# Optimization experiments

Measured on AMD Instinct MI355X. Metric: run time of the kernel, lower is better.

The kernel has to match this reference:

```python
import jax, jax.numpy as jnp
import numpy as np

N = 50000  # num nodes
E = 800000  # num edges


def gcn_layer(x, W, b, senders, receivers, snorm, rnorm):
    # jraph.GraphConvolution(Dense, add_self_edges=False, symmetric_normalization=True)
    h = x @ W + b                       # [N, F_out] dense transform
    h = h * snorm[:, None]              # scale by rsqrt(max(sender_degree, 1))
    agg = jax.ops.segment_sum(h[senders], receivers, num_segments=N)  # scatter-add over edges
    return agg * rnorm[:, None]         # scale by rsqrt(max(receiver_degree, 1))


def setup_inputs() -> dict:
    key = jax.random.key(0)
    ks = jax.random.split(key, 6)
    nodes = jax.random.normal(ks[0], (N, 128), jnp.float32)
    senders = jax.random.randint(ks[1], (E,), 0, N)
    receivers = jax.random.randint(ks[2], (E,), 0, N)

    def dense(k, fin, fout):
        kw, _ = jax.random.split(k)
        scale = 1.0 / np.sqrt(fin).astype(np.float32)
        W = jax.random.uniform(kw, (fin, fout), jnp.float32, -scale, scale)
        b = jnp.zeros((fout,), jnp.float32)
        return W, b

    W1, b1 = dense(ks[3], 128, 256)
    W2, b2 = dense(ks[4], 256, 256)
    W3, b3 = dense(ks[5], 256, 128)
    return dict(nodes=nodes, senders=senders, receivers=receivers,
                W1=W1, b1=b1, W2=W2, b2=b2, W3=W3, b3=b3)


def reference(nodes, senders, receivers, W1, b1, W2, b2, W3, b3):
    ones = jnp.ones((E,), nodes.dtype)
    sdeg = jax.ops.segment_sum(ones, senders, num_segments=N)
    rdeg = jax.ops.segment_sum(ones, receivers, num_segments=N)
    snorm = jax.lax.rsqrt(jnp.maximum(sdeg, 1.0))
    rnorm = jax.lax.rsqrt(jnp.maximum(rdeg, 1.0))

    x = nodes
    for W, b in ((W1, b1), (W2, b2), (W3, b3)):
        x = gcn_layer(x, W, b, senders, receivers, snorm, rnorm)
        x = jax.nn.relu(x)  # activation applied after every layer, incl. last
        # dropout is deterministic (eval mode) -> identity
    return x
```

## Files before the change

### kernel.cpp

```cpp
#include <hip/hip_runtime.h>
#include <hip/hip_fp16.h>


typedef __attribute__((ext_vector_type(8))) short short8;
typedef __attribute__((ext_vector_type(4))) float f32x4;

#define DCAP 64
#define PBITS 8
#define EPB 4096

static __device__ __forceinline__ float reluf(float x){ return x > 0.f ? x : 0.f; }

static __device__ __forceinline__ unsigned short bf16_rn(float v){
    unsigned u = __float_as_uint(v);
    unsigned r = u + 0x7FFFu + ((u >> 16) & 1u);
    return (unsigned short)(r >> 16);
}
static __device__ __forceinline__ void split2(float v, unsigned short& h, unsigned short& l){
    unsigned short hh = bf16_rn(v);
    float hf = __uint_as_float(((unsigned)hh) << 16);
    h = hh;
    l = bf16_rn(v - hf);
}
static __device__ __forceinline__ unsigned short f2h(float v){
    return __half_as_ushort(__float2half(v));
}
static __device__ __forceinline__ float h2f(unsigned short u){
    return __half2float(__ushort_as_half(u));
}

static __device__ __forceinline__ void gload_lds16(const void* g, void* lds){
    __builtin_amdgcn_global_load_lds((const __attribute__((address_space(1))) unsigned int*)g,
                                     (__attribute__((address_space(3))) unsigned int*)lds, 16, 0, 0);
}


__global__ __launch_bounds__(256)
void p1_hist(const int* __restrict__ snd, const int* __restrict__ rcv,
             int* __restrict__ cntR, int* __restrict__ cntS, int e, int NP, int NB)
{
    __shared__ int hR[256], hS[256];
    int t = threadIdx.x;
    hR[t] = 0; hS[t] = 0;
    __syncthreads();
    int base = blockIdx.x * EPB;
#pragma unroll
    for (int k = 0; k < EPB / 256; ++k) {
        int i = base + k * 256 + t;
        if (i < e) {
            atomicAdd(&hR[rcv[i] >> PBITS], 1);
            atomicAdd(&hS[snd[i] >> PBITS], 1);
        }
    }
    __syncthreads();
    if (t < NP) {
        cntR[t * NB + blockIdx.x] = hR[t];
        cntS[t * NB + blockIdx.x] = hS[t];
    }
}

__global__ __launch_bounds__(256)
void p2a_scanpart(const int* __restrict__ cntR, int* __restrict__ withinR, int* __restrict__ totR,
                  const int* __restrict__ cntS, int* __restrict__ withinS, int* __restrict__ totS,
                  int NB)
{
    __shared__ int s[256];
    int t = threadIdx.x;
    int p = blockIdx.x;
    int v = (t < NB) ? cntR[p * NB + t] : 0;
    s[t] = v;
    __syncthreads();
    for (int d = 1; d < 256; d <<= 1) {
        int x = (t >= d) ? s[t - d] : 0;
        __syncthreads();
        s[t] += x;
        __syncthreads();
    }
    if (t < NB) withinR[p * NB + t] = s[t] - v;
    if (t == 255) totR[p] = s[255];
    __syncthreads();
    v = (t < NB) ? cntS[p * NB + t] : 0;
    s[t] = v;
    __syncthreads();
    for (int d = 1; d < 256; d <<= 1) {
        int x = (t >= d) ? s[t - d] : 0;
        __syncthreads();
        s[t] += x;
        __syncthreads();
    }
    if (t < NB) withinS[p * NB + t] = s[t] - v;
    if (t == 255) totS[p] = s[255];
}

__global__ __launch_bounds__(256)
void p2b_scantops(const int* __restrict__ totR, int* __restrict__ pbaseR,
                  const int* __restrict__ totS, int* __restrict__ pbaseS, int NP)
{
    __shared__ int s[256];
    int t = threadIdx.x;
    int v = (t < NP) ? totR[t] : 0;
    s[t] = v;
    __syncthreads();
    for (int d = 1; d < 256; d <<= 1) {
        int x = (t >= d) ? s[t - d] : 0;
        __syncthreads();
        s[t] += x;
        __syncthreads();
    }
    if (t < NP) pbaseR[t] = s[t] - v;
    if (t == 255) pbaseR[NP] = s[255];
    __syncthreads();
    v = (t < NP) ? totS[t] : 0;
    s[t] = v;
    __syncthreads();
    for (int d = 1; d < 256; d <<= 1) {
        int x = (t >= d) ? s[t - d] : 0;
        __syncthreads();
        s[t] += x;
        __syncthreads();
    }
    if (t < NP) pbaseS[t] = s[t] - v;
    if (t == 255) pbaseS[NP] = s[255];
}

__global__ __launch_bounds__(256)
void p3_scatter(const int* __restrict__ snd, const int* __restrict__ rcv,
                const int* __restrict__ pbaseR, const int* __restrict__ withinR,
                const int* __restrict__ pbaseS, const int* __restrict__ withinS,
                unsigned int* __restrict__ eP, unsigned short* __restrict__ sP,
                int e, int NP, int NB)
{
    __shared__ int bR[256], cR[256], bS[256], cS[256];
    int t = threadIdx.x;
    if (t < NP) {
        bR[t] = pbaseR[t] + withinR[t * NB + blockIdx.x];
        bS[t] = pbaseS[t] + withinS[t * NB + blockIdx.x];
    }
    cR[t] = 0; cS[t] = 0;
    __syncthreads();
    int base = blockIdx.x * EPB;
#pragma unroll
    for (int k = 0; k < EPB / 256; ++k) {
        int i = base + k * 256 + t;
        if (i < e) {
            int s = snd[i], r = rcv[i];
            int pr = r >> PBITS, ps = s >> PBITS;
            int rk = atomicAdd(&cR[pr], 1);
            eP[bR[pr] + rk] = ((unsigned)r << 16) | (unsigned)s;
            int sk = atomicAdd(&cS[ps], 1);
            sP[bS[ps] + sk] = (unsigned short)s;
        }
    }
}

__global__ __launch_bounds__(256)
void p4_csr(const unsigned int* __restrict__ eP, const int* __restrict__ pbaseR,
            unsigned short* __restrict__ esrc, int* __restrict__ rcntP,
            float* __restrict__ rnormP, int* __restrict__ inv, int n)
{
    __shared__ unsigned short buck[256 * DCAP];
    __shared__ int cnt[256];
    __shared__ int hist[64], hbase[64], cur[64], sc[64];
    int t = threadIdx.x;
    cnt[t] = 0;
    if (t < 64) { hist[t] = 0; cur[t] = 0; }
    __syncthreads();
    int p = blockIdx.x;
    int lo = pbaseR[p];
    int hi = pbaseR[p + 1];
    for (int i = lo + t; i < hi; i += 256) {
        unsigned u = eP[i];
        int lr = (u >> 16) & 255;
        int slot = atomicAdd(&cnt[lr], 1);
        if (slot < DCAP) buck[lr * DCAP + slot] = (unsigned short)(u & 0xFFFFu);
    }
    __syncthreads();
    int nvalid = min(256, n - p * 256);
    int deg = (t < nvalid) ? min(cnt[t], 63) : -1;
    if (deg >= 0) atomicAdd(&hist[deg], 1);
    __syncthreads();
    int hv = (t < 64) ? hist[t] : 0;
    if (t < 64) sc[t] = hv;
    __syncthreads();
    for (int d = 1; d < 64; d <<= 1) {
        int x = (t < 64 && t >= d) ? sc[t - d] : 0;
        __syncthreads();
        if (t < 64) sc[t] += x;
        __syncthreads();
    }
    if (t < 64) hbase[t] = sc[t] - hv;
    __syncthreads();
    if (deg >= 0) {
        int slot = p * 256 + hbase[deg] + atomicAdd(&cur[deg], 1);
        inv[p * 256 + t] = slot;
        int full = cnt[t];
        rcntP[slot] = min(full, DCAP);
        rnormP[slot] = rsqrtf(fmaxf((float)full, 1.0f));
        unsigned short* dst = esrc + (size_t)slot * DCAP;
        const unsigned short* src = buck + t * DCAP;
#pragma unroll
        for (int k = 0; k < DCAP / 8; ++k)
            *(short8*)(dst + k * 8) = *(const short8*)(src + k * 8);
    }
}

__global__ __launch_bounds__(256)
void p4b_sdeg(const unsigned short* __restrict__ sP, const int* __restrict__ pbaseS,
              float* __restrict__ snormN, int n)
{
    __shared__ int cnt[256];
    int t = threadIdx.x;
    cnt[t] = 0;
    __syncthreads();
    int p = blockIdx.x;
    int lo = pbaseS[p];
    int hi = pbaseS[p + 1];
    for (int i = lo + t; i < hi; i += 256)
        atomicAdd(&cnt[sP[i] & 255], 1);
    __syncthreads();
    int g = p * 256 + t;
    if (g < n) snormN[g] = rsqrtf(fmaxf((float)cnt[t], 1.0f));
}

__global__ __launch_bounds__(256)
void p5_remap(unsigned short* __restrict__ esrc, const int* __restrict__ rcntP,
              const int* __restrict__ inv, const float* __restrict__ snormN,
              float* __restrict__ snormP, int n)
{
    int i = blockIdx.x * 256 + threadIdx.x;
    if (i < n) snormP[inv[i]] = snormN[i];
    if (i < n * DCAP) {
        int slot = i >> 6, j = i & 63;
        if (j < rcntP[slot]) esrc[i] = (unsigned short)inv[esrc[i]];
    }
}

__global__ void conv_h_kernel(const float* __restrict__ x, unsigned short* __restrict__ y,
                              const int* __restrict__ inv, int n)
{
    int i = blockIdx.x * 256 + threadIdx.x;
    if (i >= n * 32) return;
    int node = i >> 5, c4 = i & 31;
    float4 v = *(const float4*)(x + (size_t)node * 128 + c4 * 4);
    ushort4 o = make_ushort4(f2h(v.x), f2h(v.y), f2h(v.z), f2h(v.w));
    *(ushort4*)(y + (size_t)inv[node] * 128 + c4 * 4) = o;
}

__global__ void wsplit_kernel(const float* __restrict__ W, unsigned short* __restrict__ Th,
                              unsigned short* __restrict__ Tl, int K, int N)
{
    int i = blockIdx.x * 256 + threadIdx.x;
    if (i >= K * N) return;
    int k = i / N, c = i % N;
    unsigned short h, l;
    split2(W[i], h, l);
    Th[c * K + k] = h;
    Tl[c * K + k] = l;
}

template<int K, int NOUT, int OMODE, bool APAIR>
__global__ __launch_bounds__(256)
void mfma_gemm(const unsigned short* __restrict__ A_g,
               const unsigned short* __restrict__ Bh_g, const unsigned short* __restrict__ Bl_g,
               const float* __restrict__ bias, const float* __restrict__ rs,
               const float* __restrict__ bs, float* __restrict__ Ht,
               unsigned short* __restrict__ Ot, int n)
{
    __shared__ unsigned short smem[4 * 128 * 32];
    unsigned short* Ah = smem;
    unsigned short* Al = smem + 4096;
    unsigned short* Bh = smem + 8192;
    unsigned short* Bl = smem + 12288;

    const int tid = threadIdx.x;
    const int wid = tid >> 6, lane = tid & 63;
    const int wr = (wid >> 1) * 64, wc = (wid & 1) * 64;
    const int r0 = blockIdx.x * 128, c0 = blockIdx.y * 128;

    f32x4 acc[4][4];
#pragma unroll
    for (int m = 0; m < 4; ++m)
#pragma unroll
        for (int q = 0; q < 4; ++q) acc[m][q] = (f32x4){0.f, 0.f, 0.f, 0.f};

    const int ks = lane >> 4, lr = lane & 15;
    const int ASTRIDE = APAIR ? 2 * K : K;

    for (int k0 = 0; k0 < K; k0 += 32) {
#pragma unroll
        for (int c = 0; c < 2; ++c) {
            int i = tid + c * 256;
            int row = i >> 2, p = i & 3;
            int g = p ^ ((row >> 1) & 3);
            int ar = r0 + row; if (ar >= n) ar = n - 1;
            size_t aoff = (size_t)ar * ASTRIDE + k0 + g * 8;
            gload_lds16(A_g + aoff, Ah + i * 8);
            if (APAIR) gload_lds16(A_g + aoff + K, Al + i * 8);
            size_t boff = (size_t)(c0 + row) * K + k0 + g * 8;
            gload_lds16(Bh_g + boff, Bh + i * 8);
            gload_lds16(Bl_g + boff, Bl + i * 8);
        }
        __syncthreads();

        short8 a_h[4], a_l[4], b_h[4], b_l[4];
#pragma unroll
        for (int m = 0; m < 4; ++m) {
            int r = wr + m * 16 + lr;
            int slot = ks ^ ((r >> 1) & 3);
            a_h[m] = *(const short8*)(Ah + r * 32 + slot * 8);
            if (APAIR) a_l[m] = *(const short8*)(Al + r * 32 + slot * 8);
        }
#pragma unroll
        for (int q = 0; q < 4; ++q) {
            int r = wc + q * 16 + lr;
            int slot = ks ^ ((r >> 1) & 3);
            b_h[q] = *(const short8*)(Bh + r * 32 + slot * 8);
            b_l[q] = *(const short8*)(Bl + r * 32 + slot * 8);
        }
#pragma unroll
        for (int m = 0; m < 4; ++m)
#pragma unroll
            for (int q = 0; q < 4; ++q) {
                acc[m][q] = __builtin_amdgcn_mfma_f32_16x16x32_bf16(a_h[m], b_h[q], acc[m][q], 0, 0, 0);
                acc[m][q] = __builtin_amdgcn_mfma_f32_16x16x32_bf16(a_h[m], b_l[q], acc[m][q], 0, 0, 0);
                if (APAIR)
                    acc[m][q] = __builtin_amdgcn_mfma_f32_16x16x32_bf16(a_l[m], b_h[q], acc[m][q], 0, 0, 0);
            }
        __syncthreads();
    }

    const int lq = lane >> 4;
    float* eps = (float*)smem;
    unsigned short* eph = smem;
    unsigned short* epl = smem + 32 * 136;

#pragma unroll
    for (int m = 0; m < 4; ++m) {
        __syncthreads();
#pragma unroll
        for (int j = 0; j < 4; ++j) {
            int gr = r0 + wr + m * 16 + lq * 4 + j;
            int cr = (wid >> 1) * 16 + lq * 4 + j;
            float rsv, bsv;
            if (gr < n) { rsv = rs[gr]; bsv = bs[gr]; } else { rsv = 0.f; bsv = 0.f; }
#pragma unroll
            for (int q = 0; q < 4; ++q) {
                int col = wc + q * 16 + lr;
                float v = acc[m][q][j] * rsv + bias[c0 + col] * bsv;
                if (OMODE == 1) {
                    v = reluf(v);
                    unsigned short h, l;
                    split2(v, h, l);
                    eph[cr * 136 + col] = h;
                    epl[cr * 136 + col] = l;
                } else if (OMODE == 2) {
                    eph[cr * 136 + col] = f2h(v);
                } else if (OMODE == 3) {
                    eph[cr * 136 + col] = bf16_rn(reluf(v));
                } else {
                    eps[cr * 132 + col] = v;
                }
            }
        }
        __syncthreads();
        int rr = tid >> 3, seg = tid & 7;
        int gr = r0 + (rr >> 4) * 64 + m * 16 + (rr & 15);
        if (gr < n) {
            if (OMODE == 1) {
                unsigned short* dst = Ot + (size_t)gr * (2 * NOUT) + c0 + seg * 16;
#pragma unroll
                for (int k = 0; k < 2; ++k) {
                    *(short8*)(dst + k * 8) = *(const short8*)(eph + rr * 136 + seg * 16 + k * 8);
                    *(short8*)(dst + NOUT + k * 8) = *(const short8*)(epl + rr * 136 + seg * 16 + k * 8);
                }
            } else if (OMODE == 2 || OMODE == 3) {
                unsigned short* dst = Ot + (size_t)gr * NOUT + c0 + seg * 16;
#pragma unroll
                for (int k = 0; k < 2; ++k)
                    *(short8*)(dst + k * 8) = *(const short8*)(eph + rr * 136 + seg * 16 + k * 8);
            } else {
                float* dst = Ht + (size_t)gr * NOUT + c0 + seg * 16;
#pragma unroll
                for (int k = 0; k < 4; ++k)
                    *(float4*)(dst + k * 4) = *(const float4*)(eps + rr * 132 + seg * 16 + k * 4);
            }
        }
    }
}


__global__ __launch_bounds__(256)
void gather1_t(const unsigned short* __restrict__ Nh, const int* __restrict__ rcntP,
               const unsigned short* __restrict__ esrc, const float* __restrict__ snormP,
               const float* __restrict__ rnormP,
               unsigned short* __restrict__ G, float* __restrict__ bs, int n)
{
    int g = blockIdx.x * 256 + threadIdx.x;
    int node = g >> 4, lane = g & 15;
    if (node >= n) return;
    int col = blockIdx.y * 64 + lane * 4;
    const unsigned short* Nc = Nh + col;
    int e0 = node * DCAP;
    int e1 = e0 + rcntP[node];
    float a0 = 0, a1 = 0, a2 = 0, a3 = 0, gs = 0;
    int e = e0;
    for (; e + 4 <= e1; e += 4) {
        int s0 = esrc[e], s1 = esrc[e + 1], s2 = esrc[e + 2], s3 = esrc[e + 3];
        float n0 = snormP[s0], n1 = snormP[s1], n2 = snormP[s2], n3 = snormP[s3];
        ushort4 v0 = *(const ushort4*)(Nc + (size_t)s0 * 128);
        ushort4 v1 = *(const ushort4*)(Nc + (size_t)s1 * 128);
        ushort4 v2 = *(const ushort4*)(Nc + (size_t)s2 * 128);
        ushort4 v3 = *(const ushort4*)(Nc + (size_t)s3 * 128);
        a0 += h2f(v0.x) * n0 + h2f(v1.x) * n1 + h2f(v2.x) * n2 + h2f(v3.x) * n3;
        a1 += h2f(v0.y) * n0 + h2f(v1.y) * n1 + h2f(v2.y) * n2 + h2f(v3.y) * n3;
        a2 += h2f(v0.z) * n0 + h2f(v1.z) * n1 + h2f(v2.z) * n2 + h2f(v3.z) * n3;
        a3 += h2f(v0.w) * n0 + h2f(v1.w) * n1 + h2f(v2.w) * n2 + h2f(v3.w) * n3;
        gs += n0 + n1 + n2 + n3;
    }
    for (; e < e1; ++e) {
        int s = esrc[e];
        float ns = snormP[s];
        ushort4 v = *(const ushort4*)(Nc + (size_t)s * 128);
        a0 += h2f(v.x) * ns; a1 += h2f(v.y) * ns; a2 += h2f(v.z) * ns; a3 += h2f(v.w) * ns;
        gs += ns;
    }
    ushort4 o = make_ushort4(bf16_rn(a0), bf16_rn(a1), bf16_rn(a2), bf16_rn(a3));
    *(ushort4*)(G + (size_t)node * 128 + col) = o;
    if (blockIdx.y == 0 && lane == 0) bs[node] = gs * rnormP[node];
}

__global__ __launch_bounds__(256)
void gather2_t(const unsigned short* __restrict__ Hh, const int* __restrict__ rcntP,
               const unsigned short* __restrict__ esrc, const float* __restrict__ rnormP,
               unsigned short* __restrict__ X3, int n)
{
    int g = blockIdx.x * 256 + threadIdx.x;
    int node = g >> 4, lane = g & 15;
    if (node >= n) return;
    int col = blockIdx.y * 64 + lane * 4;
    const unsigned short* Hc = Hh + col;
    int e0 = node * DCAP;
    int e1 = e0 + rcntP[node];
    float a0 = 0, a1 = 0, a2 = 0, a3 = 0;
    int e = e0;
    for (; e + 4 <= e1; e += 4) {
        int s0 = esrc[e], s1 = esrc[e + 1], s2 = esrc[e + 2], s3 = esrc[e + 3];
        ushort4 v0 = *(const ushort4*)(Hc + (size_t)s0 * 256);
        ushort4 v1 = *(const ushort4*)(Hc + (size_t)s1 * 256);
        ushort4 v2 = *(const ushort4*)(Hc + (size_t)s2 * 256);
        ushort4 v3 = *(const ushort4*)(Hc + (size_t)s3 * 256);
        a0 += h2f(v0.x) + h2f(v1.x) + h2f(v2.x) + h2f(v3.x);
        a1 += h2f(v0.y) + h2f(v1.y) + h2f(v2.y) + h2f(v3.y);
        a2 += h2f(v0.z) + h2f(v1.z) + h2f(v2.z) + h2f(v3.z);
        a3 += h2f(v0.w) + h2f(v1.w) + h2f(v2.w) + h2f(v3.w);
    }
    for (; e < e1; ++e) {
        int s = esrc[e];
        ushort4 v = *(const ushort4*)(Hc + (size_t)s * 256);
        a0 += h2f(v.x); a1 += h2f(v.y); a2 += h2f(v.z); a3 += h2f(v.w);
    }
    float rn = rnormP[node];
    ushort4 o = make_ushort4(bf16_rn(reluf(a0 * rn)), bf16_rn(reluf(a1 * rn)),
                             bf16_rn(reluf(a2 * rn)), bf16_rn(reluf(a3 * rn)));
    *(ushort4*)(X3 + (size_t)node * 256 + col) = o;
}

__global__ __launch_bounds__(256)
void gather3_t(const unsigned short* __restrict__ Hh, const int* __restrict__ rcntP,
               const unsigned short* __restrict__ esrc, const float* __restrict__ rnormP,
               const int* __restrict__ inv, float* __restrict__ out, int n)
{
    int g = blockIdx.x * 256 + threadIdx.x;
    int node = g >> 4, lane = g & 15;
    if (node >= n) return;
    int iv = inv[node];
    int col = blockIdx.y * 64 + lane * 4;
    const unsigned short* Hc = Hh + col;
    int e0 = iv * DCAP;
    int e1 = e0 + rcntP[iv];
    float a0 = 0, a1 = 0, a2 = 0, a3 = 0;
    int e = e0;
    for (; e + 4 <= e1; e += 4) {
        int s0 = esrc[e], s1 = esrc[e + 1], s2 = esrc[e + 2], s3 = esrc[e + 3];
        ushort4 v0 = *(const ushort4*)(Hc + (size_t)s0 * 128);
        ushort4 v1 = *(const ushort4*)(Hc + (size_t)s1 * 128);
        ushort4 v2 = *(const ushort4*)(Hc + (size_t)s2 * 128);
        ushort4 v3 = *(const ushort4*)(Hc + (size_t)s3 * 128);
        a0 += h2f(v0.x) + h2f(v1.x) + h2f(v2.x) + h2f(v3.x);
        a1 += h2f(v0.y) + h2f(v1.y) + h2f(v2.y) + h2f(v3.y);
        a2 += h2f(v0.z) + h2f(v1.z) + h2f(v2.z) + h2f(v3.z);
        a3 += h2f(v0.w) + h2f(v1.w) + h2f(v2.w) + h2f(v3.w);
    }
    for (; e < e1; ++e) {
        int s = esrc[e];
        ushort4 v = *(const ushort4*)(Hc + (size_t)s * 128);
        a0 += h2f(v.x); a1 += h2f(v.y); a2 += h2f(v.z); a3 += h2f(v.w);
    }
    float rn = rnormP[iv];
    float4 o = { reluf(a0 * rn), reluf(a1 * rn), reluf(a2 * rn), reluf(a3 * rn) };
    *(float4*)(out + (size_t)node * 128 + col) = o;
}


extern "C" void kernel_launch(void* const* d_in, const int* in_sizes, int n_in,
                              void* d_out, int out_size, void* d_ws, size_t ws_size,
                              hipStream_t stream)
{
    const float* nodes = (const float*)d_in[0];
    const int*   snd   = (const int*)d_in[1];
    const int*   rcv   = (const int*)d_in[2];
    const float* W1    = (const float*)d_in[3];
    const float* b1    = (const float*)d_in[4];
    const float* W2    = (const float*)d_in[5];
    const float* b2    = (const float*)d_in[6];
    const float* W3    = (const float*)d_in[7];
    const float* b3    = (const float*)d_in[8];
    const int n = in_sizes[0] / 128;
    const int e = in_sizes[1];
    float* out = (float*)d_out;

    const int NP = (n + 255) >> 8;
    const int NB = (e + EPB - 1) / EPB;

    char* w = (char*)d_ws;
    size_t o = 0;
    auto alloc = [&](size_t b){ size_t p = o; o += (b + 255) & ~(size_t)255; return p; };
    unsigned short* Hh   = (unsigned short*)(w + alloc((size_t)n * 256 * 2));
    unsigned short* X2   = (unsigned short*)(w + alloc((size_t)n * 256 * 2));
    char*           bufA = w + alloc((size_t)n * 512 * 2);
    unsigned short* Nh   = (unsigned short*)bufA;
    unsigned short* G    = (unsigned short*)(bufA + (size_t)n * 128 * 2);
    unsigned short* X3   = (unsigned short*)bufA;
    unsigned short* Wt1h = (unsigned short*)(w + alloc(256 * 128 * 2));
    unsigned short* Wt1l = (unsigned short*)(w + alloc(256 * 128 * 2));
    unsigned short* Wt2h = (unsigned short*)(w + alloc(256 * 256 * 2));
    unsigned short* Wt2l = (unsigned short*)(w + alloc(256 * 256 * 2));
    unsigned short* Wt3h = (unsigned short*)(w + alloc(128 * 256 * 2));
    unsigned short* Wt3l = (unsigned short*)(w + alloc(128 * 256 * 2));
    float* bsb   = (float*)(w + alloc((size_t)n * 4));
    int*   cntR   = (int*)(w + alloc((size_t)NP * NB * 4));
    int*   withinR= (int*)(w + alloc((size_t)NP * NB * 4));
    int*   cntS   = (int*)(w + alloc((size_t)NP * NB * 4));
    int*   withinS= (int*)(w + alloc((size_t)NP * NB * 4));
    int*   totR   = (int*)(w + alloc((size_t)NP * 4));
    int*   totS   = (int*)(w + alloc((size_t)NP * 4));
    int*   pbaseR = (int*)(w + alloc((size_t)(NP + 1) * 4));
    int*   pbaseS = (int*)(w + alloc((size_t)(NP + 1) * 4));
    unsigned int*   eP   = (unsigned int*)  (w + alloc((size_t)e * 4));
    unsigned short* sP   = (unsigned short*)(w + alloc((size_t)e * 2));
    unsigned short* esrc = (unsigned short*)(w + alloc((size_t)n * DCAP * 2));
    int*   rcntP = (int*)  (w + alloc((size_t)n * 4));
    int*   inv   = (int*)  (w + alloc((size_t)n * 4));
    float* snormN= (float*)(w + alloc((size_t)n * 4));
    float* snormP= (float*)(w + alloc((size_t)n * 4));
    float* rnormP= (float*)(w + alloc((size_t)n * 4));

    p1_hist<<<NB, 256, 0, stream>>>(snd, rcv, cntR, cntS, e, NP, NB);
    p2a_scanpart<<<NP, 256, 0, stream>>>(cntR, withinR, totR, cntS, withinS, totS, NB);
    p2b_scantops<<<1, 256, 0, stream>>>(totR, pbaseR, totS, pbaseS, NP);
    p3_scatter<<<NB, 256, 0, stream>>>(snd, rcv, pbaseR, withinR, pbaseS, withinS, eP, sP, e, NP, NB);
    p4_csr<<<NP, 256, 0, stream>>>(eP, pbaseR, esrc, rcntP, rnormP, inv, n);
    p4b_sdeg<<<NP, 256, 0, stream>>>(sP, pbaseS, snormN, n);
    p5_remap<<<((size_t)n * DCAP + 255) / 256, 256, 0, stream>>>(esrc, rcntP, inv, snormN, snormP, n);

    conv_h_kernel<<<((size_t)n * 32 + 255) / 256, 256, 0, stream>>>(nodes, Nh, inv, n);
    wsplit_kernel<<<(128 * 256 + 255) / 256, 256, 0, stream>>>(W1, Wt1h, Wt1l, 128, 256);
    wsplit_kernel<<<(256 * 256 + 255) / 256, 256, 0, stream>>>(W2, Wt2h, Wt2l, 256, 256);
    wsplit_kernel<<<(256 * 128 + 255) / 256, 256, 0, stream>>>(W3, Wt3h, Wt3l, 256, 128);

    int gb = (n + 127) / 128;
    int lb = ((size_t)n * 16 + 255) / 256;

    gather1_t<<<dim3(lb, 2), 256, 0, stream>>>(Nh, rcntP, esrc, snormP, rnormP, G, bsb, n);
    mfma_gemm<128, 256, 3, false><<<dim3(gb, 2), 256, 0, stream>>>(G, Wt1h, Wt1l, b1, rnormP, bsb,
                                                                   (float*)nullptr, X2, n);
    mfma_gemm<256, 256, 2, false><<<dim3(gb, 2), 256, 0, stream>>>(X2, Wt2h, Wt2l, b2, snormP, snormP,
                                                                   (float*)nullptr, Hh, n);
    gather2_t<<<dim3(lb, 4), 256, 0, stream>>>(Hh, rcntP, esrc, rnormP, X3, n);
    mfma_gemm<256, 128, 2, false><<<dim3(gb, 1), 256, 0, stream>>>(X3, Wt3h, Wt3l, b3, snormP, snormP,
                                                                   (float*)nullptr, Hh, n);
    gather3_t<<<dim3(lb, 2), 256, 0, stream>>>(Hh, rcntP, esrc, rnormP, inv, out, n);
}
```

Measured before the change: 267.0 us.

## Fuse preprocessing kernels and widen gathers to 16-byte loads per lane

Folds the sender-degree pass into the CSR build kernel, merges the fp32-to-half node conversion into the remap kernel, and combines the three weight-split launches into one, cutting kernel launch count. The three gather kernels now load 8 halfs per lane with short8 instead of 4, so each lane covers twice the columns and the grid's y dimension is halved or removed. This lowers launch overhead and repeated index/norm loads per edge, but gives fewer threads in flight to hide gather latency.

```diff
diff --git a/kernel.cpp b/kernel.cpp
--- a/kernel.cpp
+++ b/kernel.cpp
@@ -155,8 +155,10 @@
 
 __global__ __launch_bounds__(256)
 void p4_csr(const unsigned int* __restrict__ eP, const int* __restrict__ pbaseR,
+            const unsigned short* __restrict__ sP, const int* __restrict__ pbaseS,
             unsigned short* __restrict__ esrc, int* __restrict__ rcntP,
-            float* __restrict__ rnormP, int* __restrict__ inv, int n)
+            float* __restrict__ rnormP, int* __restrict__ inv,
+            float* __restrict__ snormN, int n)
 {
     __shared__ unsigned short buck[256 * DCAP];
     __shared__ int cnt[256];
@@ -177,6 +179,7 @@
     __syncthreads();
     int nvalid = min(256, n - p * 256);
     int deg = (t < nvalid) ? min(cnt[t], 63) : -1;
+    int full = (t < nvalid) ? cnt[t] : 0;
     if (deg >= 0) atomicAdd(&hist[deg], 1);
     __syncthreads();
     int hv = (t < 64) ? hist[t] : 0;
@@ -193,7 +196,6 @@
     if (deg >= 0) {
         int slot = p * 256 + hbase[deg] + atomicAdd(&cur[deg], 1);
         inv[p * 256 + t] = slot;
-        int full = cnt[t];
         rcntP[slot] = min(full, DCAP);
         rnormP[slot] = rsqrtf(fmaxf((float)full, 1.0f));
         unsigned short* dst = esrc + (size_t)slot * DCAP;
@@ -202,58 +204,53 @@
         for (int k = 0; k < DCAP / 8; ++k)
             *(short8*)(dst + k * 8) = *(const short8*)(src + k * 8);
     }
-}
-
-__global__ __launch_bounds__(256)
-void p4b_sdeg(const unsigned short* __restrict__ sP, const int* __restrict__ pbaseS,
-              float* __restrict__ snormN, int n)
-{
-    __shared__ int cnt[256];
-    int t = threadIdx.x;
+    __syncthreads();
     cnt[t] = 0;
     __syncthreads();
-    int p = blockIdx.x;
-    int lo = pbaseS[p];
-    int hi = pbaseS[p + 1];
-    for (int i = lo + t; i < hi; i += 256)
+    int lo2 = pbaseS[p];
+    int hi2 = pbaseS[p + 1];
+    for (int i = lo2 + t; i < hi2; i += 256)
         atomicAdd(&cnt[sP[i] & 255], 1);
     __syncthreads();
-    int g = p * 256 + t;
-    if (g < n) snormN[g] = rsqrtf(fmaxf((float)cnt[t], 1.0f));
-}
-
-__global__ __launch_bounds__(256)
-void p5_remap(unsigned short* __restrict__ esrc, const int* __restrict__ rcntP,
-              const int* __restrict__ inv, const float* __restrict__ snormN,
-              float* __restrict__ snormP, int n)
+    if (t < nvalid) snormN[p * 256 + t] = rsqrtf(fmaxf((float)cnt[t], 1.0f));
+}
+
+__global__ __launch_bounds__(256)
+void p5_finish(unsigned short* __restrict__ esrc, const int* __restrict__ rcntP,
+               const int* __restrict__ inv, const float* __restrict__ snormN,
+               float* __restrict__ snormP, const float* __restrict__ nodes,
+               unsigned short* __restrict__ Nh, int n)
 {
     int i = blockIdx.x * 256 + threadIdx.x;
     if (i < n) snormP[inv[i]] = snormN[i];
+    if (i < n * 32) {
+        int node = i >> 5, c4 = i & 31;
+        float4 v = *(const float4*)(nodes + (size_t)node * 128 + c4 * 4);
+        ushort4 o = make_ushort4(f2h(v.x), f2h(v.y), f2h(v.z), f2h(v.w));
+        *(ushort4*)(Nh + (size_t)inv[node] * 128 + c4 * 4) = o;
+    }
     if (i < n * DCAP) {
         int slot = i >> 6, j = i & 63;
         if (j < rcntP[slot]) esrc[i] = (unsigned short)inv[esrc[i]];
     }
 }
 
-__global__ void conv_h_kernel(const float* __restrict__ x, unsigned short* __restrict__ y,
-                              const int* __restrict__ inv, int n)
+__global__ __launch_bounds__(256)
+void wsplit_all(const float* __restrict__ W1, const float* __restrict__ W2,
+                const float* __restrict__ W3,
+                unsigned short* __restrict__ T1h, unsigned short* __restrict__ T1l,
+                unsigned short* __restrict__ T2h, unsigned short* __restrict__ T2l,
+                unsigned short* __restrict__ T3h, unsigned short* __restrict__ T3l)
 {
     int i = blockIdx.x * 256 + threadIdx.x;
-    if (i >= n * 32) return;
-    int node = i >> 5, c4 = i & 31;
-    float4 v = *(const float4*)(x + (size_t)node * 128 + c4 * 4);
-    ushort4 o = make_ushort4(f2h(v.x), f2h(v.y), f2h(v.z), f2h(v.w));
-    *(ushort4*)(y + (size_t)inv[node] * 128 + c4 * 4) = o;
-}
-
-__global__ void wsplit_kernel(const float* __restrict__ W, unsigned short* __restrict__ Th,
-                              unsigned short* __restrict__ Tl, int K, int N)
-{
-    int i = blockIdx.x * 256 + threadIdx.x;
-    if (i >= K * N) return;
-    int k = i / N, c = i % N;
+    const float* W; unsigned short *Th, *Tl; int K, N, idx;
+    if (i < 32768)       { W = W1; Th = T1h; Tl = T1l; K = 128; N = 256; idx = i; }
+    else if (i < 98304)  { W = W2; Th = T2h; Tl = T2l; K = 256; N = 256; idx = i - 32768; }
+    else if (i < 131072) { W = W3; Th = T3h; Tl = T3l; K = 256; N = 128; idx = i - 98304; }
+    else return;
+    int k = idx / N, c = idx % N;
     unsigned short h, l;
-    split2(W[i], h, l);
+    split2(W[idx], h, l);
     Th[c * K + k] = h;
     Tl[c * K + k] = l;
 }
@@ -398,35 +395,39 @@
     int g = blockIdx.x * 256 + threadIdx.x;
     int node = g >> 4, lane = g & 15;
     if (node >= n) return;
-    int col = blockIdx.y * 64 + lane * 4;
+    int col = lane * 8;
     const unsigned short* Nc = Nh + col;
     int e0 = node * DCAP;
     int e1 = e0 + rcntP[node];
-    float a0 = 0, a1 = 0, a2 = 0, a3 = 0, gs = 0;
+    float a[8] = {0, 0, 0, 0, 0, 0, 0, 0};
+    float gs = 0;
     int e = e0;
     for (; e + 4 <= e1; e += 4) {
         int s0 = esrc[e], s1 = esrc[e + 1], s2 = esrc[e + 2], s3 = esrc[e + 3];
         float n0 = snormP[s0], n1 = snormP[s1], n2 = snormP[s2], n3 = snormP[s3];
-        ushort4 v0 = *(const ushort4*)(Nc + (size_t)s0 * 128);
-        ushort4 v1 = *(const ushort4*)(Nc + (size_t)s1 * 128);
-        ushort4 v2 = *(const ushort4*)(Nc + (size_t)s2 * 128);
-        ushort4 v3 = *(const ushort4*)(Nc + (size_t)s3 * 128);
-        a0 += h2f(v0.x) * n0 + h2f(v1.x) * n1 + h2f(v2.x) * n2 + h2f(v3.x) * n3;
-        a1 += h2f(v0.y) * n0 + h2f(v1.y) * n1 + h2f(v2.y) * n2 + h2f(v3.y) * n3;
-        a2 += h2f(v0.z) * n0 + h2f(v1.z) * n1 + h2f(v2.z) * n2 + h2f(v3.z) * n3;
-        a3 += h2f(v0.w) * n0 + h2f(v1.w) * n1 + h2f(v2.w) * n2 + h2f(v3.w) * n3;
+        short8 v0 = *(const short8*)(Nc + (size_t)s0 * 128);
+        short8 v1 = *(const short8*)(Nc + (size_t)s1 * 128);
+        short8 v2 = *(const short8*)(Nc + (size_t)s2 * 128);
+        short8 v3 = *(const short8*)(Nc + (size_t)s3 * 128);
+#pragma unroll
+        for (int k = 0; k < 8; ++k)
+            a[k] += h2f((unsigned short)v0[k]) * n0 + h2f((unsigned short)v1[k]) * n1
+                  + h2f((unsigned short)v2[k]) * n2 + h2f((unsigned short)v3[k]) * n3;
         gs += n0 + n1 + n2 + n3;
     }
     for (; e < e1; ++e) {
         int s = esrc[e];
         float ns = snormP[s];
-        ushort4 v = *(const ushort4*)(Nc + (size_t)s * 128);
-        a0 += h2f(v.x) * ns; a1 += h2f(v.y) * ns; a2 += h2f(v.z) * ns; a3 += h2f(v.w) * ns;
+        short8 v = *(const short8*)(Nc + (size_t)s * 128);
+#pragma unroll
+        for (int k = 0; k < 8; ++k) a[k] += h2f((unsigned short)v[k]) * ns;
         gs += ns;
     }
-    ushort4 o = make_ushort4(bf16_rn(a0), bf16_rn(a1), bf16_rn(a2), bf16_rn(a3));
-    *(ushort4*)(G + (size_t)node * 128 + col) = o;
-    if (blockIdx.y == 0 && lane == 0) bs[node] = gs * rnormP[node];
+    short8 o;
+#pragma unroll
+    for (int k = 0; k < 8; ++k) o[k] = (short)bf16_rn(a[k]);
+    *(short8*)(G + (size_t)node * 128 + col) = o;
+    if (lane == 0) bs[node] = gs * rnormP[node];
 }
 
 __global__ __launch_bounds__(256)
@@ -437,32 +438,34 @@
     int g = blockIdx.x * 256 + threadIdx.x;
     int node = g >> 4, lane = g & 15;
     if (node >= n) return;
-    int col = blockIdx.y * 64 + lane * 4;
+    int col = blockIdx.y * 128 + lane * 8;
     const unsigned short* Hc = Hh + col;
     int e0 = node * DCAP;
     int e1 = e0 + rcntP[node];
-    float a0 = 0, a1 = 0, a2 = 0, a3 = 0;
+    float a[8] = {0, 0, 0, 0, 0, 0, 0, 0};
     int e = e0;
     for (; e + 4 <= e1; e += 4) {
         int s0 = esrc[e], s1 = esrc[e + 1], s2 = esrc[e + 2], s3 = esrc[e + 3];
-        ushort4 v0 = *(const ushort4*)(Hc + (size_t)s0 * 256);
-        ushort4 v1 = *(const ushort4*)(Hc + (size_t)s1 * 256);
-        ushort4 v2 = *(const ushort4*)(Hc + (size_t)s2 * 256);
-        ushort4 v3 = *(const ushort4*)(Hc + (size_t)s3 * 256);
-        a0 += h2f(v0.x) + h2f(v1.x) + h2f(v2.x) + h2f(v3.x);
-        a1 += h2f(v0.y) + h2f(v1.y) + h2f(v2.y) + h2f(v3.y);
-        a2 += h2f(v0.z) + h2f(v1.z) + h2f(v2.z) + h2f(v3.z);
-        a3 += h2f(v0.w) + h2f(v1.w) + h2f(v2.w) + h2f(v3.w);
+        short8 v0 = *(const short8*)(Hc + (size_t)s0 * 256);
+        short8 v1 = *(const short8*)(Hc + (size_t)s1 * 256);
+        short8 v2 = *(const short8*)(Hc + (size_t)s2 * 256);
+        short8 v3 = *(const short8*)(Hc + (size_t)s3 * 256);
+#pragma unroll
+        for (int k = 0; k < 8; ++k)
+            a[k] += h2f((unsigned short)v0[k]) + h2f((unsigned short)v1[k])
+                  + h2f((unsigned short)v2[k]) + h2f((unsigned short)v3[k]);
     }
     for (; e < e1; ++e) {
         int s = esrc[e];
-        ushort4 v = *(const ushort4*)(Hc + (size_t)s * 256);
-        a0 += h2f(v.x); a1 += h2f(v.y); a2 += h2f(v.z); a3 += h2f(v.w);
+        short8 v = *(const short8*)(Hc + (size_t)s * 256);
+#pragma unroll
+        for (int k = 0; k < 8; ++k) a[k] += h2f((unsigned short)v[k]);
     }
     float rn = rnormP[node];
-    ushort4 o = make_ushort4(bf16_rn(reluf(a0 * rn)), bf16_rn(reluf(a1 * rn)),
-                             bf16_rn(reluf(a2 * rn)), bf16_rn(reluf(a3 * rn)));
-    *(ushort4*)(X3 + (size_t)node * 256 + col) = o;
+    short8 o;
+#pragma unroll
+    for (int k = 0; k < 8; ++k) o[k] = (short)bf16_rn(reluf(a[k] * rn));
+    *(short8*)(X3 + (size_t)node * 256 + col) = o;
 }
 
 __global__ __launch_bounds__(256)
@@ -474,31 +477,35 @@
     int node = g >> 4, lane = g & 15;
     if (node >= n) return;
     int iv = inv[node];
-    int col = blockIdx.y * 64 + lane * 4;
+    int col = lane * 8;
     const unsigned short* Hc = Hh + col;
     int e0 = iv * DCAP;
     int e1 = e0 + rcntP[iv];
-    float a0 = 0, a1 = 0, a2 = 0, a3 = 0;
+    float a[8] = {0, 0, 0, 0, 0, 0, 0, 0};
     int e = e0;
     for (; e + 4 <= e1; e += 4) {
         int s0 = esrc[e], s1 = esrc[e + 1], s2 = esrc[e + 2], s3 = esrc[e + 3];
-        ushort4 v0 = *(const ushort4*)(Hc + (size_t)s0 * 128);
-        ushort4 v1 = *(const ushort4*)(Hc + (size_t)s1 * 128);
-        ushort4 v2 = *(const ushort4*)(Hc + (size_t)s2 * 128);
-        ushort4 v3 = *(const ushort4*)(Hc + (size_t)s3 * 128);
-        a0 += h2f(v0.x) + h2f(v1.x) + h2f(v2.x) + h2f(v3.x);
-        a1 += h2f(v0.y) + h2f(v1.y) + h2f(v2.y) + h2f(v3.y);
-        a2 += h2f(v0.z) + h2f(v1.z) + h2f(v2.z) + h2f(v3.z);
-        a3 += h2f(v0.w) + h2f(v1.w) + h2f(v2.w) + h2f(v3.w);
+        short8 v0 = *(const short8*)(Hc + (size_t)s0 * 128);
+        short8 v1 = *(const short8*)(Hc + (size_t)s1 * 128);
+        short8 v2 = *(const short8*)(Hc + (size_t)s2 * 128);
+        short8 v3 = *(const short8*)(Hc + (size_t)s3 * 128);
+#pragma unroll
+        for (int k = 0; k < 8; ++k)
+            a[k] += h2f((unsigned short)v0[k]) + h2f((unsigned short)v1[k])
+                  + h2f((unsigned short)v2[k]) + h2f((unsigned short)v3[k]);
     }
     for (; e < e1; ++e) {
         int s = esrc[e];
-        ushort4 v = *(const ushort4*)(Hc + (size_t)s * 128);
-        a0 += h2f(v.x); a1 += h2f(v.y); a2 += h2f(v.z); a3 += h2f(v.w);
+        short8 v = *(const short8*)(Hc + (size_t)s * 128);
+#pragma unroll
+        for (int k = 0; k < 8; ++k) a[k] += h2f((unsigned short)v[k]);
     }
     float rn = rnormP[iv];
-    float4 o = { reluf(a0 * rn), reluf(a1 * rn), reluf(a2 * rn), reluf(a3 * rn) };
-    *(float4*)(out + (size_t)node * 128 + col) = o;
+    float* dst = out + (size_t)node * 128 + col;
+    float4 o0 = { reluf(a[0] * rn), reluf(a[1] * rn), reluf(a[2] * rn), reluf(a[3] * rn) };
+    float4 o1 = { reluf(a[4] * rn), reluf(a[5] * rn), reluf(a[6] * rn), reluf(a[7] * rn) };
+    *(float4*)dst = o0;
+    *(float4*)(dst + 4) = o1;
 }
 
 
@@ -559,25 +566,21 @@
     p2a_scanpart<<<NP, 256, 0, stream>>>(cntR, withinR, totR, cntS, withinS, totS, NB);
     p2b_scantops<<<1, 256, 0, stream>>>(totR, pbaseR, totS, pbaseS, NP);
     p3_scatter<<<NB, 256, 0, stream>>>(snd, rcv, pbaseR, withinR, pbaseS, withinS, eP, sP, e, NP, NB);
-    p4_csr<<<NP, 256, 0, stream>>>(eP, pbaseR, esrc, rcntP, rnormP, inv, n);
-    p4b_sdeg<<<NP, 256, 0, stream>>>(sP, pbaseS, snormN, n);
-    p5_remap<<<((size_t)n * DCAP + 255) / 256, 256, 0, stream>>>(esrc, rcntP, inv, snormN, snormP, n);
-
-    conv_h_kernel<<<((size_t)n * 32 + 255) / 256, 256, 0, stream>>>(nodes, Nh, inv, n);
-    wsplit_kernel<<<(128 * 256 + 255) / 256, 256, 0, stream>>>(W1, Wt1h, Wt1l, 128, 256);
-    wsplit_kernel<<<(256 * 256 + 255) / 256, 256, 0, stream>>>(W2, Wt2h, Wt2l, 256, 256);
-    wsplit_kernel<<<(256 * 128 + 255) / 256, 256, 0, stream>>>(W3, Wt3h, Wt3l, 256, 128);
+    p4_csr<<<NP, 256, 0, stream>>>(eP, pbaseR, sP, pbaseS, esrc, rcntP, rnormP, inv, snormN, n);
+    p5_finish<<<((size_t)n * DCAP + 255) / 256, 256, 0, stream>>>(esrc, rcntP, inv, snormN, snormP,
+                                                                  nodes, Nh, n);
+    wsplit_all<<<512, 256, 0, stream>>>(W1, W2, W3, Wt1h, Wt1l, Wt2h, Wt2l, Wt3h, Wt3l);
 
     int gb = (n + 127) / 128;
     int lb = ((size_t)n * 16 + 255) / 256;
 
-    gather1_t<<<dim3(lb, 2), 256, 0, stream>>>(Nh, rcntP, esrc, snormP, rnormP, G, bsb, n);
+    gather1_t<<<lb, 256, 0, stream>>>(Nh, rcntP, esrc, snormP, rnormP, G, bsb, n);
     mfma_gemm<128, 256, 3, false><<<dim3(gb, 2), 256, 0, stream>>>(G, Wt1h, Wt1l, b1, rnormP, bsb,
                                                                    (float*)nullptr, X2, n);
     mfma_gemm<256, 256, 2, false><<<dim3(gb, 2), 256, 0, stream>>>(X2, Wt2h, Wt2l, b2, snormP, snormP,
                                                                    (float*)nullptr, Hh, n);
-    gather2_t<<<dim3(lb, 4), 256, 0, stream>>>(Hh, rcntP, esrc, rnormP, X3, n);
+    gather2_t<<<dim3(lb, 2), 256, 0, stream>>>(Hh, rcntP, esrc, rnormP, X3, n);
     mfma_gemm<256, 128, 2, false><<<dim3(gb, 1), 256, 0, stream>>>(X3, Wt3h, Wt3l, b3, snormP, snormP,
                                                                    (float*)nullptr, Hh, n);
-    gather3_t<<<dim3(lb, 2), 256, 0, stream>>>(Hh, rcntP, esrc, rnormP, inv, out, n);
-}
+    gather3_t<<<lb, 256, 0, stream>>>(Hh, rcntP, esrc, rnormP, inv, out, n);
+}
```

After: 258.6 us. 3.1% less time.
